# Kernel optimization log

Measured on AMD Instinct MI355X. Metric: run time of the kernel, lower is better.

Reference implementation:

```python
import jax, jax.numpy as jnp
import numpy as np

EMB = 512
HEADS = 8
USE_MASK = True


def setup_inputs() -> dict:
    key = jax.random.key(0)
    ks = jax.random.split(key, 6)
    b, t, e, h = 4, 1024, EMB, HEADS
    scale = 1.0 / np.sqrt(e)
    return {
        "x": jax.random.normal(ks[0], (b, t, e), dtype=jnp.float32),
        # nn.Linear(emb, emb*heads, bias=False) weights, stored as (out, in) like torch
        "w_k": jax.random.normal(ks[1], (e * h, e), dtype=jnp.float32) * scale,
        "w_q": jax.random.normal(ks[2], (e * h, e), dtype=jnp.float32) * scale,
        "w_v": jax.random.normal(ks[3], (e * h, e), dtype=jnp.float32) * scale,
        # unifyheads: Linear(heads*emb, emb) with bias
        "w_u": jax.random.normal(ks[4], (e, e * h), dtype=jnp.float32) * (1.0 / np.sqrt(e * h)),
        "b_u": jax.random.normal(ks[5], (e,), dtype=jnp.float32) * 0.01,
    }


def _attention(x, w_k, w_q, w_v, w_u, b_u):
    b, t, e = x.shape
    h = HEADS
    # projections: (b,t,e) @ (e, e*h) -> (b,t,h,e)  (per-head dim == emb, 'wide' heads)
    k = (x @ w_k.T).reshape(b, t, h, e)
    q = (x @ w_q.T).reshape(b, t, h, e)
    v = (x @ w_v.T).reshape(b, t, h, e)
    # scale q and k each by e^{-1/4} (equiv. to scores / sqrt(e))
    s = e ** (-0.25)
    q = q * s
    k = k * s
    # scores: (b,h,t,t)
    dot = jnp.einsum("bqhe,bkhe->bhqk", q, k)
    if USE_MASK:
        # mask strictly-upper triangle (future positions), diagonal kept
        causal = jnp.tril(jnp.ones((t, t), dtype=bool))
        dot = jnp.where(causal, dot, -jnp.inf)
    attn = jax.nn.softmax(dot, axis=-1)
    out = jnp.einsum("bhqk,bkhe->bqhe", attn, v).reshape(b, t, h * e)
    return out @ w_u.T + b_u


def reference(x, w_k, w_q, w_v, w_u, b_u):
    return _attention(x, w_k, w_q, w_v, w_u, b_u)
```

## Files before the change

### kernel.cpp

```cpp
#include <hip/hip_runtime.h>
#include <stdint.h>

typedef unsigned short u16;
typedef unsigned int u32;
typedef __bf16 bf16_t;
typedef __attribute__((ext_vector_type(8))) bf16_t bf16x8;
typedef __attribute__((ext_vector_type(4))) float floatx4;

__device__ __forceinline__ u16 f2b(float f) {
  u32 u = __float_as_uint(f);
  return (u16)((u + 0x7fffu + ((u >> 16) & 1u)) >> 16);
}

__device__ __forceinline__ void gload_lds16(const u16* g, u16* l) {
  __builtin_amdgcn_global_load_lds(
      (const __attribute__((address_space(1))) u32*)g,
      (__attribute__((address_space(3))) u32*)l, 16, 0, 0);
}

__global__ __launch_bounds__(256) void cvt_kernel(
    const float* __restrict__ s0, const float* __restrict__ s1,
    const float* __restrict__ s2, const float* __restrict__ s3,
    const float* __restrict__ s4, u16* __restrict__ dbase) {
  const int which = blockIdx.y;
  const float* s = which == 0 ? s0 : which == 1 ? s1 : which == 2 ? s2
                 : which == 3 ? s3 : s4;
  u16* d = dbase + (long)which * 2097152;
  const int i = blockIdx.x * 256 + threadIdx.x;
  const float4 v = ((const float4*)s)[i];
  ushort4 o;
  o.x = f2b(v.x); o.y = f2b(v.y); o.z = f2b(v.z); o.w = f2b(v.w);
  ((ushort4*)d)[i] = o;
}

__global__ __launch_bounds__(256) void init_out_kernel(float* __restrict__ out,
                                                       const float* __restrict__ bias) {
  const int i = blockIdx.x * 256 + threadIdx.x;
  const int c4 = i & 127;
  ((float4*)out)[i] = ((const float4*)bias)[c4];
}

enum { A_PLAIN = 0, A_HEADBLK = 1 };
enum { B_PLAIN = 0, B_TRANS = 1 };
enum { C_BF16_PLAIN = 0, C_BF16_BHTE = 1, C_F32_PLAIN = 2, C_F32_ATOMIC = 3 };

#define MFMA16(MB)                                                                                 \
  do {                                                                                             \
    acc[(MB) + 0][0] = __builtin_amdgcn_mfma_f32_16x16x32_bf16(A0, B0, acc[(MB) + 0][0], 0, 0, 0); \
    acc[(MB) + 0][1] = __builtin_amdgcn_mfma_f32_16x16x32_bf16(A0, B1, acc[(MB) + 0][1], 0, 0, 0); \
    acc[(MB) + 0][2] = __builtin_amdgcn_mfma_f32_16x16x32_bf16(A0, B2, acc[(MB) + 0][2], 0, 0, 0); \
    acc[(MB) + 0][3] = __builtin_amdgcn_mfma_f32_16x16x32_bf16(A0, B3, acc[(MB) + 0][3], 0, 0, 0); \
    acc[(MB) + 1][0] = __builtin_amdgcn_mfma_f32_16x16x32_bf16(A1, B0, acc[(MB) + 1][0], 0, 0, 0); \
    acc[(MB) + 1][1] = __builtin_amdgcn_mfma_f32_16x16x32_bf16(A1, B1, acc[(MB) + 1][1], 0, 0, 0); \
    acc[(MB) + 1][2] = __builtin_amdgcn_mfma_f32_16x16x32_bf16(A1, B2, acc[(MB) + 1][2], 0, 0, 0); \
    acc[(MB) + 1][3] = __builtin_amdgcn_mfma_f32_16x16x32_bf16(A1, B3, acc[(MB) + 1][3], 0, 0, 0); \
    acc[(MB) + 2][0] = __builtin_amdgcn_mfma_f32_16x16x32_bf16(A2, B0, acc[(MB) + 2][0], 0, 0, 0); \
    acc[(MB) + 2][1] = __builtin_amdgcn_mfma_f32_16x16x32_bf16(A2, B1, acc[(MB) + 2][1], 0, 0, 0); \
    acc[(MB) + 2][2] = __builtin_amdgcn_mfma_f32_16x16x32_bf16(A2, B2, acc[(MB) + 2][2], 0, 0, 0); \
    acc[(MB) + 2][3] = __builtin_amdgcn_mfma_f32_16x16x32_bf16(A2, B3, acc[(MB) + 2][3], 0, 0, 0); \
    acc[(MB) + 3][0] = __builtin_amdgcn_mfma_f32_16x16x32_bf16(A3, B0, acc[(MB) + 3][0], 0, 0, 0); \
    acc[(MB) + 3][1] = __builtin_amdgcn_mfma_f32_16x16x32_bf16(A3, B1, acc[(MB) + 3][1], 0, 0, 0); \
    acc[(MB) + 3][2] = __builtin_amdgcn_mfma_f32_16x16x32_bf16(A3, B2, acc[(MB) + 3][2], 0, 0, 0); \
    acc[(MB) + 3][3] = __builtin_amdgcn_mfma_f32_16x16x32_bf16(A3, B3, acc[(MB) + 3][3], 0, 0, 0); \
  } while (0)

#define STG_A(hn, c)                                                             \
  {                                                                              \
    const int kn_ = (hn) & 15;                                                   \
    gload_lds16(ag + (long)((c) << 7) * lda + (kn_ << 5),                        \
                &lds[(((kn_ >> 1) & 1) << 15) + ((kn_ & 1) << 13) + ((c) << 12) + ls]); \
  }
#define STG_B(hn, c)                                                             \
  {                                                                              \
    const int kn_ = (hn) & 15, zn_ = (hn) >> 4;                                  \
    gload_lds16(bg + (long)zn_ * b_zstride + (long)((c) << 7) * ldb + (kn_ << 5),\
                &lds[(((kn_ >> 1) & 1) << 15) + 16384 + ((kn_ & 1) << 13) + ((c) << 12) + ls]); \
  }

#define PHASE_SYNC_PRE()                                \
  __builtin_amdgcn_s_barrier();                         \
  asm volatile("s_waitcnt lgkmcnt(0)" ::: "memory");    \
  __builtin_amdgcn_sched_barrier(0);                    \
  __builtin_amdgcn_s_setprio(1)

#define PHASE_SYNC_POST()                               \
  __builtin_amdgcn_s_setprio(0);                        \
  __builtin_amdgcn_s_barrier();                         \
  __builtin_amdgcn_sched_barrier(0)

#define HALF_ITER(kk, hn, DO_STAGE, VM)                               \
  {                                                                   \
    const int slab_ = ((((kk) >> 1) & 1) << 15) + (((kk) & 1) << 13); \
    const u16* la_ = &lds[slab_ + ard];                               \
    const u16* lb_ = &lds[slab_ + brd];                               \
    A0 = *(const bf16x8*)(la_ + 0 * 512);                             \
    A1 = *(const bf16x8*)(la_ + 1 * 512);                             \
    A2 = *(const bf16x8*)(la_ + 2 * 512);                             \
    A3 = *(const bf16x8*)(la_ + 3 * 512);                             \
    B0 = *(const bf16x8*)(lb_ + 0 * 512);                             \
    B1 = *(const bf16x8*)(lb_ + 1 * 512);                             \
    B2 = *(const bf16x8*)(lb_ + 2 * 512);                             \
    B3 = *(const bf16x8*)(lb_ + 3 * 512);                             \
    if (DO_STAGE) { STG_A((hn), 0); STG_A((hn), 1); }                 \
    PHASE_SYNC_PRE();                                                 \
    MFMA16(0);                                                        \
    PHASE_SYNC_POST();                                                \
    A0 = *(const bf16x8*)(la_ + 4 * 512);                             \
    A1 = *(const bf16x8*)(la_ + 5 * 512);                             \
    A2 = *(const bf16x8*)(la_ + 6 * 512);                             \
    A3 = *(const bf16x8*)(la_ + 7 * 512);                             \
    if (DO_STAGE) { STG_B((hn), 0); STG_B((hn), 1); }                 \
    PHASE_SYNC_PRE();                                                 \
    MFMA16(4);                                                        \
    __builtin_amdgcn_s_setprio(0);                                    \
    asm volatile("s_waitcnt vmcnt(" #VM ")" ::: "memory");            \
    __builtin_amdgcn_s_barrier();                                     \
    __builtin_amdgcn_sched_barrier(0);                                \
  }

__global__ __launch_bounds__(512, 2) void gemm256_kernel(
    const u16* __restrict__ A, int lda,
    const u16* __restrict__ B, int ldb, long b_zstride,
    u16* __restrict__ C, long c_zstride) {
  __shared__ u16 lds[65536];

  const int tid = threadIdx.x;
  const int wid = tid >> 6, lane = tid & 63;
  const int lrow = lane & 15, quad = lane >> 4;
  const int wm = wid >> 2, wn = wid & 3;

  const int o = blockIdx.x;
  const int xcd = o & 7, j = o >> 3;
  const int m0 = (((xcd >> 1) << 2) | (j >> 3)) << 8;
  const int n0 = (((xcd & 1) << 3) | (j & 7)) << 8;

  const int scol = (((lane & 3) ^ ((lane >> 3) & 3)) << 3);
  const u16* ag = A + (long)(m0 + (wid << 4) + (lane >> 2)) * lda + scol;
  const u16* bg = B + (long)(n0 + (wid << 4) + (lane >> 2)) * ldb + scol;
  const int ls = wid << 9;

  const int qsw = ((quad ^ ((lrow >> 1) & 3)) << 3);
  const int ard = (((wm << 7) + lrow) << 5) + qsw;
  const int brd = 16384 + (((wn << 6) + lrow) << 5) + qsw;

  floatx4 acc[8][4];
#pragma unroll
  for (int i = 0; i < 8; ++i)
#pragma unroll
    for (int jj = 0; jj < 4; ++jj) acc[i][jj] = (floatx4)0.0f;

  STG_A(0, 0); STG_A(0, 1); STG_B(0, 0); STG_B(0, 1);
  STG_A(1, 0); STG_A(1, 1); STG_B(1, 0); STG_B(1, 1);
  STG_A(2, 0); STG_A(2, 1); STG_B(2, 0); STG_B(2, 1);
  asm volatile("s_waitcnt vmcnt(8)" ::: "memory");
  __builtin_amdgcn_s_barrier();
  __builtin_amdgcn_sched_barrier(0);

  bf16x8 A0, A1, A2, A3, B0, B1, B2, B3;

  for (int z = 0; z < 3; ++z) {
    const int hb = z << 4;
    if (z < 2) {
      for (int kk = 0; kk < 16; ++kk) HALF_ITER(kk, hb + kk + 3, true, 8);
    } else {
      for (int kk = 0; kk < 13; ++kk) HALF_ITER(kk, hb + kk + 3, true, 8);
      HALF_ITER(13, 0, false, 4);
      HALF_ITER(14, 0, false, 0);
      {
        const int slab_ = 32768 + 8192;
        const u16* la_ = &lds[slab_ + ard];
        const u16* lb_ = &lds[slab_ + brd];
        A0 = *(const bf16x8*)(la_ + 0 * 512);
        A1 = *(const bf16x8*)(la_ + 1 * 512);
        A2 = *(const bf16x8*)(la_ + 2 * 512);
        A3 = *(const bf16x8*)(la_ + 3 * 512);
        B0 = *(const bf16x8*)(lb_ + 0 * 512);
        B1 = *(const bf16x8*)(lb_ + 1 * 512);
        B2 = *(const bf16x8*)(lb_ + 2 * 512);
        B3 = *(const bf16x8*)(lb_ + 3 * 512);
        PHASE_SYNC_PRE();
        MFMA16(0);
        PHASE_SYNC_POST();
        A0 = *(const bf16x8*)(la_ + 4 * 512);
        A1 = *(const bf16x8*)(la_ + 5 * 512);
        A2 = *(const bf16x8*)(la_ + 6 * 512);
        A3 = *(const bf16x8*)(la_ + 7 * 512);
        PHASE_SYNC_PRE();
        MFMA16(4);
        __builtin_amdgcn_s_setprio(0);
      }
    }

#pragma unroll
    for (int mi = 0; mi < 8; ++mi) {
#pragma unroll
      for (int ni = 0; ni < 4; ++ni) {
        const int cg = n0 + (wn << 6) + (ni << 4) + lrow;
        const long cbase = (long)z * c_zstride + (long)(cg >> 9) * 524288 + (cg & 511);
#pragma unroll
        for (int r = 0; r < 4; ++r) {
          const int rg = m0 + (wm << 7) + (mi << 4) + (quad << 2) + r;
          C[cbase + (long)(rg >> 10) * 4194304 + (long)(rg & 1023) * 512] = f2b(acc[mi][ni][r]);
        }
        acc[mi][ni] = (floatx4)0.0f;
      }
    }
  }
}

__global__ __launch_bounds__(256) void vt_kernel(const u16* __restrict__ V,
                                                 u16* __restrict__ VT) {
  __shared__ u16 tl[4096];
  const long base = (long)blockIdx.z * 524288;
  const int t0 = blockIdx.x << 6, e0 = blockIdx.y << 6;
  const int tid = threadIdx.x;
  const int r = tid >> 3, g = tid & 7;
#pragma unroll
  for (int h = 0; h < 2; ++h) {
    const int row = r + (h << 5);
    const uint4 v = *(const uint4*)&V[base + (long)(t0 + row) * 512 + e0 + (g << 3)];
    *(uint4*)&tl[(row << 6) + ((g ^ (row & 7)) << 3)] = v;
  }
  __syncthreads();
#pragma unroll
  for (int h = 0; h < 2; ++h) {
    const int el = r + (h << 5);
    union { u16 us[8]; uint4 v; } o;
#pragma unroll
    for (int j = 0; j < 8; ++j) {
      const int trow = (g << 3) + j;
      o.us[j] = tl[(trow << 6) + ((((el >> 3) ^ (trow & 7)) << 3) + (el & 7))];
    }
    *(uint4*)&VT[base + (long)(e0 + el) * 1024 + t0 + (g << 3)] = o.v;
  }
}

#define FS_STG(es)                                                          \
  {                                                                         \
    const int sl_ = (es) % 3;                                               \
    gload_lds16(qgq + (es) * 64, &lds[sl_ * 12288 + ls]);                   \
    gload_lds16(kgj + (es) * 64, &lds[sl_ * 12288 + 4096 + ls]);            \
    gload_lds16(kgj + (es) * 64 + 32, &lds[sl_ * 12288 + 8192 + ls]);       \
  }
#define FV_STG(c)                                                           \
  {                                                                         \
    const int vb_ = 45056 + ((c) & 1) * 16384;                              \
    const u16* vgc_ = vgj + (c) * 131072;                                   \
    gload_lds16(vgc_, &lds[vb_ + ls]);                                      \
    gload_lds16(vgc_ + 32, &lds[vb_ + 4096 + ls]);                          \
    gload_lds16(vgc_ + 64, &lds[vb_ + 8192 + ls]);                          \
    gload_lds16(vgc_ + 96, &lds[vb_ + 12288 + ls]);                         \
  }

__global__ __launch_bounds__(512, 2) void flash_kernel(
    const u16* __restrict__ Qg, const u16* __restrict__ Kg,
    const u16* __restrict__ VTg, u16* __restrict__ Og) {
  __shared__ u16 lds[77824];

  const int tid = threadIdx.x;
  const int wid = tid >> 6, lane = tid & 63;
  const int lrow = lane & 15, quad = lane >> 4;
  const int wm = wid >> 2, wn = wid & 3;

  const int blk = blockIdx.x;
  const int bh = ((blk & 7) << 2) | ((blk >> 3) & 3);
  const int pr = blk >> 5;

  const long base = (long)bh * 524288;
  const u16* Qb = Qg + base;
  const u16* Kb = Kg + base;
  const u16* Vb = VTg + base;
  u16* Ob = Og + base;

  const int scol = (((lane & 3) ^ ((lane >> 3) & 3)) << 3);
  const int ls = wid << 9;
  const int qsw = ((quad ^ ((lrow >> 1) & 3)) << 3);

  const u16* qg0 = Qb + (long)(((wid & 3) << 4) + (lane >> 2)) * 512 + ((wid >> 2) << 5) + scol;
  const u16* kg0 = Kb + (long)((wid << 4) + (lane >> 2)) * 512 + scol;
  const u16* vg0 = Vb + (long)((wid << 4) + (lane >> 2)) * 1024 + scol;

  const int a_rd = ((wm << 5) + lrow) * 32 + qsw;
  const int b_rd = ((wn << 5) + lrow) * 32 + qsw;
  const int p_rd = 36864 + ((wm << 5) + lrow) * 32 + qsw;
  float* red_max = (float*)lds;
  float* red_sum = ((float*)lds) + 256;
  const float s2 = 0.044194173824159216f;

  for (int ht = 0; ht < 2; ++ht) {
    const int qt = ht ? (15 - pr) : pr;
    const int q0 = qt << 6;
    const int nk = (qt >> 1) + 1;
    const u16* qgq = qg0 + (long)q0 * 512;

    floatx4 oa[2][4][2];
#pragma unroll
    for (int a = 0; a < 2; ++a)
#pragma unroll
      for (int b = 0; b < 4; ++b)
#pragma unroll
        for (int c = 0; c < 2; ++c) oa[a][b][c] = (floatx4)0.0f;
    float m_st[2][4], l_st[2][4];
#pragma unroll
    for (int a = 0; a < 2; ++a)
#pragma unroll
      for (int r = 0; r < 4; ++r) { m_st[a][r] = -3.0e38f; l_st[a][r] = 0.0f; }

    for (int j = 0; j < nk; ++j) {
      const int k0 = j << 7;
      const bool maskt = (j == nk - 1);
      const u16* kgj = kg0 + (long)k0 * 512;
      const u16* vgj = vg0 + k0;

      floatx4 sacc[2][2];
      sacc[0][0] = sacc[0][1] = sacc[1][0] = sacc[1][1] = (floatx4)0.0f;

      FS_STG(0); FS_STG(1);
      asm volatile("s_waitcnt vmcnt(3)" ::: "memory");
      __builtin_amdgcn_s_barrier();
      __builtin_amdgcn_sched_barrier(0);
#pragma unroll
      for (int es = 0; es < 8; ++es) {
        const int sb = (es % 3) * 12288;
        bf16x8 qa[2][2], kb[2][2];
#pragma unroll
        for (int ks = 0; ks < 2; ++ks) {
#pragma unroll
          for (int mi = 0; mi < 2; ++mi)
            qa[ks][mi] = *(const bf16x8*)&lds[sb + ks * 2048 + a_rd + mi * 512];
#pragma unroll
          for (int ni = 0; ni < 2; ++ni)
            kb[ks][ni] = *(const bf16x8*)&lds[sb + 4096 + ks * 4096 + b_rd + ni * 512];
        }
        if (es < 6) FS_STG(es + 2);
        __builtin_amdgcn_s_barrier();
        asm volatile("s_waitcnt lgkmcnt(0)" ::: "memory");
        __builtin_amdgcn_sched_barrier(0);
        __builtin_amdgcn_s_setprio(1);
#pragma unroll
        for (int ks = 0; ks < 2; ++ks)
#pragma unroll
          for (int mi = 0; mi < 2; ++mi)
#pragma unroll
            for (int ni = 0; ni < 2; ++ni)
              sacc[mi][ni] = __builtin_amdgcn_mfma_f32_16x16x32_bf16(
                  qa[ks][mi], kb[ks][ni], sacc[mi][ni], 0, 0, 0);
        __builtin_amdgcn_s_setprio(0);
        if (es < 6) { asm volatile("s_waitcnt vmcnt(3)" ::: "memory"); }
        else if (es == 6) { asm volatile("s_waitcnt vmcnt(0)" ::: "memory"); }
        __builtin_amdgcn_s_barrier();
        __builtin_amdgcn_sched_barrier(0);
      }

      FV_STG(0); FV_STG(1);

      float sv[2][2][4];
#pragma unroll
      for (int mi = 0; mi < 2; ++mi)
#pragma unroll
        for (int ni = 0; ni < 2; ++ni)
#pragma unroll
          for (int r = 0; r < 4; ++r) {
            float s = sacc[mi][ni][r] * s2;
            if (maskt) {
              const int kc = k0 + (wn << 5) + (ni << 4) + lrow;
              const int qr = q0 + (wm << 5) + (mi << 4) + (quad << 2) + r;
              if (kc > qr) s = -3.0e38f;
            }
            sv[mi][ni][r] = s;
          }
      float rm[2][4];
#pragma unroll
      for (int mi = 0; mi < 2; ++mi)
#pragma unroll
        for (int r = 0; r < 4; ++r) {
          float v = fmaxf(sv[mi][0][r], sv[mi][1][r]);
          v = fmaxf(v, __shfl_xor(v, 1));
          v = fmaxf(v, __shfl_xor(v, 2));
          v = fmaxf(v, __shfl_xor(v, 4));
          v = fmaxf(v, __shfl_xor(v, 8));
          rm[mi][r] = v;
        }
      if (lrow == 0) {
#pragma unroll
        for (int mi = 0; mi < 2; ++mi)
#pragma unroll
          for (int r = 0; r < 4; ++r)
            red_max[(((wm << 5) + (mi << 4) + (quad << 2) + r) << 2) + wn] = rm[mi][r];
      }
      asm volatile("s_waitcnt lgkmcnt(0)" ::: "memory");
      __builtin_amdgcn_s_barrier();
      float mnew[2][4], resc[2][4];
#pragma unroll
      for (int mi = 0; mi < 2; ++mi)
#pragma unroll
        for (int r = 0; r < 4; ++r) {
          const float4 v4 =
              *(const float4*)&red_max[(((wm << 5) + (mi << 4) + (quad << 2) + r) << 2)];
          const float tm = fmaxf(fmaxf(v4.x, v4.y), fmaxf(v4.z, v4.w));
          const float mn = fmaxf(m_st[mi][r], tm);
          mnew[mi][r] = mn;
          resc[mi][r] = __expf(m_st[mi][r] - mn);
          m_st[mi][r] = mn;
        }
      float ps[2][4];
#pragma unroll
      for (int mi = 0; mi < 2; ++mi)
#pragma unroll
        for (int r = 0; r < 4; ++r) {
          const float p0 = __expf(sv[mi][0][r] - mnew[mi][r]);
          const float p1 = __expf(sv[mi][1][r] - mnew[mi][r]);
          sv[mi][0][r] = p0;
          sv[mi][1][r] = p1;
          float v = p0 + p1;
          v += __shfl_xor(v, 1);
          v += __shfl_xor(v, 2);
          v += __shfl_xor(v, 4);
          v += __shfl_xor(v, 8);
          ps[mi][r] = v;
        }
      if (lrow == 0) {
#pragma unroll
        for (int mi = 0; mi < 2; ++mi)
#pragma unroll
          for (int r = 0; r < 4; ++r)
            red_sum[(((wm << 5) + (mi << 4) + (quad << 2) + r) << 2) + wn] = ps[mi][r];
      }
#pragma unroll
      for (int mi = 0; mi < 2; ++mi)
#pragma unroll
        for (int c = 0; c < 4; ++c)
#pragma unroll
          for (int n2 = 0; n2 < 2; ++n2)
#pragma unroll
            for (int r = 0; r < 4; ++r) oa[mi][c][n2][r] *= resc[mi][r];
      asm volatile("s_waitcnt lgkmcnt(0)" ::: "memory");
      __builtin_amdgcn_s_barrier();
#pragma unroll
      for (int mi = 0; mi < 2; ++mi)
#pragma unroll
        for (int r = 0; r < 4; ++r) {
          const float4 v4 =
              *(const float4*)&red_sum[(((wm << 5) + (mi << 4) + (quad << 2) + r) << 2)];
          l_st[mi][r] = l_st[mi][r] * resc[mi][r] + (v4.x + v4.y + v4.z + v4.w);
        }
#pragma unroll
      for (int mi = 0; mi < 2; ++mi)
#pragma unroll
        for (int ni = 0; ni < 2; ++ni)
#pragma unroll
          for (int r = 0; r < 4; ++r) {
            const int qrow = (wm << 5) + (mi << 4) + (quad << 2) + r;
            const int c32 = (ni << 4) + lrow;
            const int slot = (c32 >> 3) ^ ((qrow >> 1) & 3);
            lds[36864 + (wn << 11) + qrow * 32 + (slot << 3) + (c32 & 7)] =
                f2b(sv[mi][ni][r]);
          }
      asm volatile("s_waitcnt lgkmcnt(0)" ::: "memory");
      asm volatile("s_waitcnt vmcnt(4)" ::: "memory");
      __builtin_amdgcn_s_barrier();
      __builtin_amdgcn_sched_barrier(0);

      bf16x8 pa[2][4];
#pragma unroll
      for (int mi = 0; mi < 2; ++mi)
#pragma unroll
        for (int ks = 0; ks < 4; ++ks)
          pa[mi][ks] = *(const bf16x8*)&lds[p_rd + mi * 512 + ks * 2048];
#pragma unroll
      for (int c = 0; c < 4; ++c) {
        const int vb0 = 45056 + (c & 1) * 16384;
        bf16x8 vb[2][4];
#pragma unroll
        for (int n2 = 0; n2 < 2; ++n2)
#pragma unroll
          for (int ks = 0; ks < 4; ++ks)
            vb[n2][ks] = *(const bf16x8*)&lds[vb0 + ks * 4096 + b_rd + n2 * 512];
        asm volatile("s_waitcnt lgkmcnt(0)" ::: "memory");
        __builtin_amdgcn_sched_barrier(0);
        __builtin_amdgcn_s_barrier();
        if (c < 2) FV_STG(c + 2);
        __builtin_amdgcn_s_setprio(1);
#pragma unroll
        for (int ks = 0; ks < 4; ++ks)
#pragma unroll
          for (int mi = 0; mi < 2; ++mi)
#pragma unroll
            for (int n2 = 0; n2 < 2; ++n2)
              oa[mi][c][n2] = __builtin_amdgcn_mfma_f32_16x16x32_bf16(
                  pa[mi][ks], vb[n2][ks], oa[mi][c][n2], 0, 0, 0);
        __builtin_amdgcn_s_setprio(0);
        if (c < 2) { asm volatile("s_waitcnt vmcnt(4)" ::: "memory"); }
        else if (c == 2) { asm volatile("s_waitcnt vmcnt(0)" ::: "memory"); }
        __builtin_amdgcn_s_barrier();
        __builtin_amdgcn_sched_barrier(0);
      }
    }

    float inv[2][4];
#pragma unroll
    for (int mi = 0; mi < 2; ++mi)
#pragma unroll
      for (int r = 0; r < 4; ++r) inv[mi][r] = 1.0f / l_st[mi][r];
#pragma unroll
    for (int mi = 0; mi < 2; ++mi)
#pragma unroll
      for (int c = 0; c < 4; ++c)
#pragma unroll
        for (int n2 = 0; n2 < 2; ++n2)
#pragma unroll
          for (int r = 0; r < 4; ++r) {
            const int trow = q0 + (wm << 5) + (mi << 4) + (quad << 2) + r;
            const int e = (c << 7) + (wn << 5) + (n2 << 4) + lrow;
            Ob[(long)trow * 512 + e] = f2b(oa[mi][c][n2][r] * inv[mi][r]);
          }
  }
}

template <int AMODE, int BMODE, int CMODE, bool CAUSAL_SKIP, bool PV_KLIM, bool HAS_BIAS,
          bool SPLITK>
__global__ __launch_bounds__(256, 2) void gemm_kernel(
    const u16* __restrict__ A, int lda, long a_zstride,
    const u16* __restrict__ B, int ldb, long b_zstride,
    void* __restrict__ C, int ldc, long c_zstride,
    const float* __restrict__ bias, int K, float scale) {
  const int bn = blockIdx.x, bm = blockIdx.y, bz = blockIdx.z;
  if (CAUSAL_SKIP && bn > bm) return;

  int kTiles = K >> 5;
  if (PV_KLIM) kTiles = (bm + 1) * 4;
  const int kbase = SPLITK ? bz * K : 0;

  const u16* Ab = A + (SPLITK ? 0 : (long)bz * a_zstride);
  const u16* Bb = B + (SPLITK ? 0 : (long)bz * b_zstride);

  constexpr int BSTR = (BMODE == B_TRANS) ? 40 : 32;
  __shared__ u16 sA[128 * 32];
  __shared__ u16 sB[128 * BSTR];

  const int tid = threadIdx.x;
  const int wid = tid >> 6;
  const int lane = tid & 63;
  const int lrow = lane & 15;
  const int quad = lane >> 4;
  const int wm = wid >> 1, wn = wid & 1;
  const int m0 = bm * 128, n0 = bn * 128;

  const int sgr = lane >> 2;
  const int sgc = (lane & 3) << 3;

  floatx4 acc[4][4];
#pragma unroll
  for (int i = 0; i < 4; ++i)
#pragma unroll
    for (int j = 0; j < 4; ++j) acc[i][j] = (floatx4)0.0f;

  for (int kt = 0; kt < kTiles; ++kt) {
    const int k0 = kbase + (kt << 5);
#pragma unroll
    for (int j = 0; j < 2; ++j) {
      const int r = wid * 32 + j * 16 + sgr;
      const u16* g;
      if constexpr (AMODE == A_PLAIN) {
        g = Ab + (long)(m0 + r) * lda + (k0 + sgc);
      } else {
        const int rg = m0 + r, kg = k0 + sgc;
        g = Ab + (long)((rg >> 10) * 8 + (kg >> 9)) * 524288 +
            (long)(rg & 1023) * 512 + (kg & 511);
      }
      gload_lds16(g, &sA[(wid * 32 + j * 16) * 32]);
    }
    if constexpr (BMODE == B_PLAIN) {
#pragma unroll
      for (int j = 0; j < 2; ++j) {
        const int r = wid * 32 + j * 16 + sgr;
        const u16* g = Bb + (long)(n0 + r) * ldb + (k0 + sgc);
        gload_lds16(g, &sB[(wid * 32 + j * 16) * 32]);
      }
    } else {
      const int tr = tid & 31, te = (tid >> 5) << 4;
      const u16* g = Bb + (long)(k0 + tr) * ldb + (n0 + te);
      union { uint4 v[2]; u16 s[16]; } tmp;
      tmp.v[0] = *(const uint4*)g;
      tmp.v[1] = *(const uint4*)(g + 8);
#pragma unroll
      for (int i = 0; i < 16; ++i) sB[(te + i) * BSTR + tr] = tmp.s[i];
    }
    __syncthreads();

    bf16x8 af[4], bfr[4];
#pragma unroll
    for (int i = 0; i < 4; ++i)
      af[i] = *(const bf16x8*)&sA[(wm * 64 + i * 16 + lrow) * 32 + (quad << 3)];
#pragma unroll
    for (int i = 0; i < 4; ++i)
      bfr[i] = *(const bf16x8*)&sB[(wn * 64 + i * 16 + lrow) * BSTR + (quad << 3)];
#pragma unroll
    for (int mi = 0; mi < 4; ++mi)
#pragma unroll
      for (int ni = 0; ni < 4; ++ni)
        acc[mi][ni] = __builtin_amdgcn_mfma_f32_16x16x32_bf16(af[mi], bfr[ni], acc[mi][ni], 0, 0, 0);
    __syncthreads();
  }

#pragma unroll
  for (int mi = 0; mi < 4; ++mi) {
#pragma unroll
    for (int ni = 0; ni < 4; ++ni) {
      const int cg = n0 + wn * 64 + ni * 16 + lrow;
      float bv = 0.0f;
      if constexpr (HAS_BIAS) bv = bias[cg];
#pragma unroll
      for (int r = 0; r < 4; ++r) {
        const int rg = m0 + wm * 64 + mi * 16 + quad * 4 + r;
        const float val = acc[mi][ni][r] * scale + bv;
        if constexpr (CMODE == C_F32_PLAIN) {
          ((float*)C)[(long)bz * c_zstride + (long)rg * ldc + cg] = val;
        } else if constexpr (CMODE == C_F32_ATOMIC) {
          atomicAdd(&((float*)C)[(long)rg * ldc + cg], val);
        } else if constexpr (CMODE == C_BF16_PLAIN) {
          ((u16*)C)[(long)bz * c_zstride + (long)rg * ldc + cg] = f2b(val);
        } else {
          const long idx = (long)bz * c_zstride +
                           (long)((rg >> 10) * 8 + (cg >> 9)) * 524288 +
                           (long)(rg & 1023) * 512 + (cg & 511);
          ((u16*)C)[idx] = f2b(val);
        }
      }
    }
  }
}

extern "C" void kernel_launch(void* const* d_in, const int* in_sizes, int n_in,
                              void* d_out, int out_size, void* d_ws, size_t ws_size,
                              hipStream_t stream) {
  const float* x   = (const float*)d_in[0];
  const float* w_k = (const float*)d_in[1];
  const float* w_q = (const float*)d_in[2];
  const float* w_v = (const float*)d_in[3];
  const float* w_u = (const float*)d_in[4];
  const float* b_u = (const float*)d_in[5];
  float* out = (float*)d_out;
  char* ws = (char*)d_ws;

  const long MB = 1048576;
  u16* xb  = (u16*)(ws);
  u16* wqb = (u16*)(ws + 4 * MB);
  u16* wub = (u16*)(ws + 16 * MB);
  u16* Q   = (u16*)(ws + 20 * MB);
  u16* Kb  = (u16*)(ws + 52 * MB);
  u16* V   = (u16*)(ws + 84 * MB);
  u16* O   = (u16*)(ws + 116 * MB);
  u16* VT  = (u16*)(ws + 148 * MB);

  const dim3 blk(256);

  cvt_kernel<<<dim3(2048, 5), blk, 0, stream>>>(x, w_q, w_k, w_v, w_u, xb);

  gemm256_kernel<<<dim3(256), dim3(512), 0, stream>>>(
      xb, 512, wqb, 512, 2097152, Q, 16777216);

  vt_kernel<<<dim3(16, 8, 32), blk, 0, stream>>>(V, VT);

  flash_kernel<<<dim3(256), dim3(512), 0, stream>>>(Q, Kb, VT, O);

  init_out_kernel<<<2048, blk, 0, stream>>>(out, b_u);
  gemm_kernel<A_HEADBLK, B_PLAIN, C_F32_ATOMIC, false, false, false, true>
      <<<dim3(4, 32, 4), blk, 0, stream>>>(O, 0, 0, wub, 4096, 0, out, 512, 0,
                                           nullptr, 1024, 1.0f);
}
```

Baseline: 312.2 us.

## Enlarge flash attention Q tile to 128 rows and drop paired-tile scheduling

The flash kernel now processes one 128-row query tile per block, where before each block handled two 64-row tiles in a balanced pair (pr and 15-pr). Each K/V chunk loaded into LDS is now reused across twice as many query rows, and the LDS layout is reorganized with a smaller total footprint. Register pressure rises because the O accumulator and softmax state double, and causal load balance gets worse, since blocks now do between 1 and 8 key tiles. Grid size still depends on the launch code, which is not visible here.

```diff
diff --git a/kernel.cpp b/kernel.cpp
--- a/kernel.cpp
+++ b/kernel.cpp
@@ -235,27 +235,28 @@
   }
 }
 
-#define FS_STG(es)                                                          \
-  {                                                                         \
-    const int sl_ = (es) % 3;                                               \
-    gload_lds16(qgq + (es) * 64, &lds[sl_ * 12288 + ls]);                   \
-    gload_lds16(kgj + (es) * 64, &lds[sl_ * 12288 + 4096 + ls]);            \
-    gload_lds16(kgj + (es) * 64 + 32, &lds[sl_ * 12288 + 8192 + ls]);       \
-  }
-#define FV_STG(c)                                                           \
-  {                                                                         \
-    const int vb_ = 45056 + ((c) & 1) * 16384;                              \
-    const u16* vgc_ = vgj + (c) * 131072;                                   \
-    gload_lds16(vgc_, &lds[vb_ + ls]);                                      \
-    gload_lds16(vgc_ + 32, &lds[vb_ + 4096 + ls]);                          \
-    gload_lds16(vgc_ + 64, &lds[vb_ + 8192 + ls]);                          \
-    gload_lds16(vgc_ + 96, &lds[vb_ + 12288 + ls]);                         \
+#define FS3(es)                                                            \
+  {                                                                        \
+    const int sl_ = ((es) % 3) * 16384;                                    \
+    gload_lds16(qgq + (es) * 64, &lds[sl_ + ls]);                          \
+    gload_lds16(qgq + (es) * 64 + 32, &lds[sl_ + 4096 + ls]);              \
+    gload_lds16(kgj + (es) * 64, &lds[sl_ + 8192 + ls]);                   \
+    gload_lds16(kgj + (es) * 64 + 32, &lds[sl_ + 12288 + ls]);             \
+  }
+#define FV3(c)                                                             \
+  {                                                                        \
+    const int vb_ = ((c) & 1) << 14;                                       \
+    const u16* vgc_ = vgj + (c) * 131072;                                  \
+    gload_lds16(vgc_, &lds[vb_ + ls]);                                     \
+    gload_lds16(vgc_ + 32, &lds[vb_ + 4096 + ls]);                         \
+    gload_lds16(vgc_ + 64, &lds[vb_ + 8192 + ls]);                         \
+    gload_lds16(vgc_ + 96, &lds[vb_ + 12288 + ls]);                        \
   }
 
 __global__ __launch_bounds__(512, 2) void flash_kernel(
     const u16* __restrict__ Qg, const u16* __restrict__ Kg,
     const u16* __restrict__ VTg, u16* __restrict__ Og) {
-  __shared__ u16 lds[77824];
+  __shared__ u16 lds[67584];
 
   const int tid = threadIdx.x;
   const int wid = tid >> 6, lane = tid & 63;
@@ -264,7 +265,9 @@
 
   const int blk = blockIdx.x;
   const int bh = ((blk & 7) << 2) | ((blk >> 3) & 3);
-  const int pr = blk >> 5;
+  const int qt = blk >> 5;
+  const int q0 = qt << 7;
+  const int nk = qt + 1;
 
   const long base = (long)bh * 524288;
   const u16* Qb = Qg + base;
@@ -276,245 +279,235 @@
   const int ls = wid << 9;
   const int qsw = ((quad ^ ((lrow >> 1) & 3)) << 3);
 
-  const u16* qg0 = Qb + (long)(((wid & 3) << 4) + (lane >> 2)) * 512 + ((wid >> 2) << 5) + scol;
+  const u16* qgq = Qb + (long)(q0 + (wid << 4) + (lane >> 2)) * 512 + scol;
   const u16* kg0 = Kb + (long)((wid << 4) + (lane >> 2)) * 512 + scol;
   const u16* vg0 = Vb + (long)((wid << 4) + (lane >> 2)) * 1024 + scol;
 
-  const int a_rd = ((wm << 5) + lrow) * 32 + qsw;
-  const int b_rd = ((wn << 5) + lrow) * 32 + qsw;
-  const int p_rd = 36864 + ((wm << 5) + lrow) * 32 + qsw;
-  float* red_max = (float*)lds;
-  float* red_sum = ((float*)lds) + 256;
+  const int a_rd = ((wm << 6) + lrow) * 32 + qsw;
+  const int k_rd = ((wn << 5) + lrow) * 32 + qsw;
+  const int p_rd = 49152 + ((wm << 6) + lrow) * 32 + qsw;
+  float* red_max = (float*)&lds[65536];
+  float* red_sum = red_max + 512;
   const float s2 = 0.044194173824159216f;
 
-  for (int ht = 0; ht < 2; ++ht) {
-    const int qt = ht ? (15 - pr) : pr;
-    const int q0 = qt << 6;
-    const int nk = (qt >> 1) + 1;
-    const u16* qgq = qg0 + (long)q0 * 512;
-
-    floatx4 oa[2][4][2];
-#pragma unroll
-    for (int a = 0; a < 2; ++a)
-#pragma unroll
-      for (int b = 0; b < 4; ++b)
-#pragma unroll
-        for (int c = 0; c < 2; ++c) oa[a][b][c] = (floatx4)0.0f;
-    float m_st[2][4], l_st[2][4];
-#pragma unroll
-    for (int a = 0; a < 2; ++a)
-#pragma unroll
-      for (int r = 0; r < 4; ++r) { m_st[a][r] = -3.0e38f; l_st[a][r] = 0.0f; }
-
-    for (int j = 0; j < nk; ++j) {
-      const int k0 = j << 7;
-      const bool maskt = (j == nk - 1);
-      const u16* kgj = kg0 + (long)k0 * 512;
-      const u16* vgj = vg0 + k0;
-
-      floatx4 sacc[2][2];
-      sacc[0][0] = sacc[0][1] = sacc[1][0] = sacc[1][1] = (floatx4)0.0f;
-
-      FS_STG(0); FS_STG(1);
-      asm volatile("s_waitcnt vmcnt(3)" ::: "memory");
+  floatx4 oa[4][4][2];
+#pragma unroll
+  for (int a = 0; a < 4; ++a)
+#pragma unroll
+    for (int b = 0; b < 4; ++b)
+#pragma unroll
+      for (int c = 0; c < 2; ++c) oa[a][b][c] = (floatx4)0.0f;
+  float m_st[4][4], l_st[4][4];
+#pragma unroll
+  for (int a = 0; a < 4; ++a)
+#pragma unroll
+    for (int r = 0; r < 4; ++r) { m_st[a][r] = -3.0e38f; l_st[a][r] = 0.0f; }
+
+  for (int j = 0; j < nk; ++j) {
+    const int k0 = j << 7;
+    const bool mk = (j == nk - 1);
+    const u16* kgj = kg0 + (long)k0 * 512;
+    const u16* vgj = vg0 + k0;
+
+    floatx4 sacc[4][2];
+#pragma unroll
+    for (int mi = 0; mi < 4; ++mi) { sacc[mi][0] = (floatx4)0.0f; sacc[mi][1] = (floatx4)0.0f; }
+
+    FS3(0); FS3(1);
+    asm volatile("s_waitcnt vmcnt(4)" ::: "memory");
+    __builtin_amdgcn_s_barrier();
+    __builtin_amdgcn_sched_barrier(0);
+#pragma unroll
+    for (int es = 0; es < 8; ++es) {
+      const int sb = (es % 3) * 16384;
+      if (es < 6) FS3(es + 2);
       __builtin_amdgcn_s_barrier();
       __builtin_amdgcn_sched_barrier(0);
-#pragma unroll
-      for (int es = 0; es < 8; ++es) {
-        const int sb = (es % 3) * 12288;
-        bf16x8 qa[2][2], kb[2][2];
-#pragma unroll
-        for (int ks = 0; ks < 2; ++ks) {
-#pragma unroll
-          for (int mi = 0; mi < 2; ++mi)
-            qa[ks][mi] = *(const bf16x8*)&lds[sb + ks * 2048 + a_rd + mi * 512];
+      __builtin_amdgcn_s_setprio(1);
+#pragma unroll
+      for (int ks = 0; ks < 2; ++ks) {
+        bf16x8 qa[4], kb[2];
+#pragma unroll
+        for (int mi = 0; mi < 4; ++mi)
+          qa[mi] = *(const bf16x8*)&lds[sb + ks * 4096 + a_rd + mi * 512];
+#pragma unroll
+        for (int ni = 0; ni < 2; ++ni)
+          kb[ni] = *(const bf16x8*)&lds[sb + 8192 + ks * 4096 + k_rd + ni * 512];
+#pragma unroll
+        for (int mi = 0; mi < 4; ++mi)
 #pragma unroll
           for (int ni = 0; ni < 2; ++ni)
-            kb[ks][ni] = *(const bf16x8*)&lds[sb + 4096 + ks * 4096 + b_rd + ni * 512];
-        }
-        if (es < 6) FS_STG(es + 2);
-        __builtin_amdgcn_s_barrier();
-        asm volatile("s_waitcnt lgkmcnt(0)" ::: "memory");
-        __builtin_amdgcn_sched_barrier(0);
-        __builtin_amdgcn_s_setprio(1);
-#pragma unroll
-        for (int ks = 0; ks < 2; ++ks)
-#pragma unroll
-          for (int mi = 0; mi < 2; ++mi)
-#pragma unroll
-            for (int ni = 0; ni < 2; ++ni)
-              sacc[mi][ni] = __builtin_amdgcn_mfma_f32_16x16x32_bf16(
-                  qa[ks][mi], kb[ks][ni], sacc[mi][ni], 0, 0, 0);
-        __builtin_amdgcn_s_setprio(0);
-        if (es < 6) { asm volatile("s_waitcnt vmcnt(3)" ::: "memory"); }
-        else if (es == 6) { asm volatile("s_waitcnt vmcnt(0)" ::: "memory"); }
-        __builtin_amdgcn_s_barrier();
-        __builtin_amdgcn_sched_barrier(0);
-      }
-
-      FV_STG(0); FV_STG(1);
-
-      float sv[2][2][4];
-#pragma unroll
-      for (int mi = 0; mi < 2; ++mi)
-#pragma unroll
-        for (int ni = 0; ni < 2; ++ni)
-#pragma unroll
-          for (int r = 0; r < 4; ++r) {
-            float s = sacc[mi][ni][r] * s2;
-            if (maskt) {
-              const int kc = k0 + (wn << 5) + (ni << 4) + lrow;
-              const int qr = q0 + (wm << 5) + (mi << 4) + (quad << 2) + r;
-              if (kc > qr) s = -3.0e38f;
-            }
-            sv[mi][ni][r] = s;
-          }
-      float rm[2][4];
-#pragma unroll
-      for (int mi = 0; mi < 2; ++mi)
-#pragma unroll
-        for (int r = 0; r < 4; ++r) {
-          float v = fmaxf(sv[mi][0][r], sv[mi][1][r]);
-          v = fmaxf(v, __shfl_xor(v, 1));
-          v = fmaxf(v, __shfl_xor(v, 2));
-          v = fmaxf(v, __shfl_xor(v, 4));
-          v = fmaxf(v, __shfl_xor(v, 8));
-          rm[mi][r] = v;
-        }
-      if (lrow == 0) {
-#pragma unroll
-        for (int mi = 0; mi < 2; ++mi)
-#pragma unroll
-          for (int r = 0; r < 4; ++r)
-            red_max[(((wm << 5) + (mi << 4) + (quad << 2) + r) << 2) + wn] = rm[mi][r];
-      }
-      asm volatile("s_waitcnt lgkmcnt(0)" ::: "memory");
-      __builtin_amdgcn_s_barrier();
-      float mnew[2][4], resc[2][4];
-#pragma unroll
-      for (int mi = 0; mi < 2; ++mi)
-#pragma unroll
-        for (int r = 0; r < 4; ++r) {
-          const float4 v4 =
-              *(const float4*)&red_max[(((wm << 5) + (mi << 4) + (quad << 2) + r) << 2)];
-          const float tm = fmaxf(fmaxf(v4.x, v4.y), fmaxf(v4.z, v4.w));
-          const float mn = fmaxf(m_st[mi][r], tm);
-          mnew[mi][r] = mn;
-          resc[mi][r] = __expf(m_st[mi][r] - mn);
-          m_st[mi][r] = mn;
-        }
-      float ps[2][4];
-#pragma unroll
-      for (int mi = 0; mi < 2; ++mi)
-#pragma unroll
-        for (int r = 0; r < 4; ++r) {
-          const float p0 = __expf(sv[mi][0][r] - mnew[mi][r]);
-          const float p1 = __expf(sv[mi][1][r] - mnew[mi][r]);
-          sv[mi][0][r] = p0;
-          sv[mi][1][r] = p1;
-          float v = p0 + p1;
-          v += __shfl_xor(v, 1);
-          v += __shfl_xor(v, 2);
-          v += __shfl_xor(v, 4);
-          v += __shfl_xor(v, 8);
-          ps[mi][r] = v;
-        }
-      if (lrow == 0) {
-#pragma unroll
-        for (int mi = 0; mi < 2; ++mi)
-#pragma unroll
-          for (int r = 0; r < 4; ++r)
-            red_sum[(((wm << 5) + (mi << 4) + (quad << 2) + r) << 2) + wn] = ps[mi][r];
-      }
-#pragma unroll
-      for (int mi = 0; mi < 2; ++mi)
-#pragma unroll
-        for (int c = 0; c < 4; ++c)
-#pragma unroll
-          for (int n2 = 0; n2 < 2; ++n2)
-#pragma unroll
-            for (int r = 0; r < 4; ++r) oa[mi][c][n2][r] *= resc[mi][r];
-      asm volatile("s_waitcnt lgkmcnt(0)" ::: "memory");
-      __builtin_amdgcn_s_barrier();
-#pragma unroll
-      for (int mi = 0; mi < 2; ++mi)
-#pragma unroll
-        for (int r = 0; r < 4; ++r) {
-          const float4 v4 =
-              *(const float4*)&red_sum[(((wm << 5) + (mi << 4) + (quad << 2) + r) << 2)];
-          l_st[mi][r] = l_st[mi][r] * resc[mi][r] + (v4.x + v4.y + v4.z + v4.w);
-        }
-#pragma unroll
-      for (int mi = 0; mi < 2; ++mi)
-#pragma unroll
-        for (int ni = 0; ni < 2; ++ni)
-#pragma unroll
-          for (int r = 0; r < 4; ++r) {
-            const int qrow = (wm << 5) + (mi << 4) + (quad << 2) + r;
-            const int c32 = (ni << 4) + lrow;
-            const int slot = (c32 >> 3) ^ ((qrow >> 1) & 3);
-            lds[36864 + (wn << 11) + qrow * 32 + (slot << 3) + (c32 & 7)] =
-                f2b(sv[mi][ni][r]);
-          }
-      asm volatile("s_waitcnt lgkmcnt(0)" ::: "memory");
-      asm volatile("s_waitcnt vmcnt(4)" ::: "memory");
+            sacc[mi][ni] = __builtin_amdgcn_mfma_f32_16x16x32_bf16(
+                qa[mi], kb[ni], sacc[mi][ni], 0, 0, 0);
+      }
+      __builtin_amdgcn_s_setprio(0);
+      if (es < 6) { asm volatile("s_waitcnt vmcnt(4)" ::: "memory"); }
+      else if (es == 6) { asm volatile("s_waitcnt vmcnt(0)" ::: "memory"); }
       __builtin_amdgcn_s_barrier();
       __builtin_amdgcn_sched_barrier(0);
-
-      bf16x8 pa[2][4];
-#pragma unroll
-      for (int mi = 0; mi < 2; ++mi)
+    }
+
+    FV3(0); FV3(1);
+
+    float sv[4][2][4];
+#pragma unroll
+    for (int mi = 0; mi < 4; ++mi)
+#pragma unroll
+      for (int ni = 0; ni < 2; ++ni)
+#pragma unroll
+        for (int r = 0; r < 4; ++r) {
+          float s = sacc[mi][ni][r] * s2;
+          if (mk) {
+            const int kc = k0 + (wn << 5) + (ni << 4) + lrow;
+            const int qr = q0 + (wm << 6) + (mi << 4) + (quad << 2) + r;
+            if (kc > qr) s = -3.0e38f;
+          }
+          sv[mi][ni][r] = s;
+        }
+    float rm[4][4];
+#pragma unroll
+    for (int mi = 0; mi < 4; ++mi)
+#pragma unroll
+      for (int r = 0; r < 4; ++r) {
+        float v = fmaxf(sv[mi][0][r], sv[mi][1][r]);
+        v = fmaxf(v, __shfl_xor(v, 1));
+        v = fmaxf(v, __shfl_xor(v, 2));
+        v = fmaxf(v, __shfl_xor(v, 4));
+        v = fmaxf(v, __shfl_xor(v, 8));
+        rm[mi][r] = v;
+      }
+    if (lrow == 0) {
+#pragma unroll
+      for (int mi = 0; mi < 4; ++mi)
+#pragma unroll
+        for (int r = 0; r < 4; ++r)
+          red_max[(((wm << 6) + (mi << 4) + (quad << 2) + r) << 2) + wn] = rm[mi][r];
+    }
+    asm volatile("s_waitcnt lgkmcnt(0)" ::: "memory");
+    __builtin_amdgcn_s_barrier();
+    float mnew[4][4], resc[4][4];
+#pragma unroll
+    for (int mi = 0; mi < 4; ++mi)
+#pragma unroll
+      for (int r = 0; r < 4; ++r) {
+        const float4 v4 =
+            *(const float4*)&red_max[(((wm << 6) + (mi << 4) + (quad << 2) + r) << 2)];
+        const float tm = fmaxf(fmaxf(v4.x, v4.y), fmaxf(v4.z, v4.w));
+        const float mn = fmaxf(m_st[mi][r], tm);
+        mnew[mi][r] = mn;
+        resc[mi][r] = __expf(m_st[mi][r] - mn);
+        m_st[mi][r] = mn;
+      }
+    float ps[4][4];
+#pragma unroll
+    for (int mi = 0; mi < 4; ++mi)
+#pragma unroll
+      for (int r = 0; r < 4; ++r) {
+        const float p0 = __expf(sv[mi][0][r] - mnew[mi][r]);
+        const float p1 = __expf(sv[mi][1][r] - mnew[mi][r]);
+        sv[mi][0][r] = p0;
+        sv[mi][1][r] = p1;
+        float v = p0 + p1;
+        v += __shfl_xor(v, 1);
+        v += __shfl_xor(v, 2);
+        v += __shfl_xor(v, 4);
+        v += __shfl_xor(v, 8);
+        ps[mi][r] = v;
+      }
+    if (lrow == 0) {
+#pragma unroll
+      for (int mi = 0; mi < 4; ++mi)
+#pragma unroll
+        for (int r = 0; r < 4; ++r)
+          red_sum[(((wm << 6) + (mi << 4) + (quad << 2) + r) << 2) + wn] = ps[mi][r];
+    }
+#pragma unroll
+    for (int mi = 0; mi < 4; ++mi)
+#pragma unroll
+      for (int c = 0; c < 4; ++c)
+#pragma unroll
+        for (int n2 = 0; n2 < 2; ++n2)
+#pragma unroll
+          for (int r = 0; r < 4; ++r) oa[mi][c][n2][r] *= resc[mi][r];
+    asm volatile("s_waitcnt lgkmcnt(0)" ::: "memory");
+    __builtin_amdgcn_s_barrier();
+#pragma unroll
+    for (int mi = 0; mi < 4; ++mi)
+#pragma unroll
+      for (int r = 0; r < 4; ++r) {
+        const float4 v4 =
+            *(const float4*)&red_sum[(((wm << 6) + (mi << 4) + (quad << 2) + r) << 2)];
+        l_st[mi][r] = l_st[mi][r] * resc[mi][r] + (v4.x + v4.y + v4.z + v4.w);
+      }
+#pragma unroll
+    for (int mi = 0; mi < 4; ++mi)
+#pragma unroll
+      for (int ni = 0; ni < 2; ++ni)
+#pragma unroll
+        for (int r = 0; r < 4; ++r) {
+          const int qrow = (wm << 6) + (mi << 4) + (quad << 2) + r;
+          const int c32 = (ni << 4) + lrow;
+          const int slot = (c32 >> 3) ^ ((qrow >> 1) & 3);
+          lds[49152 + (wn << 12) + qrow * 32 + (slot << 3) + (c32 & 7)] =
+              f2b(sv[mi][ni][r]);
+        }
+    asm volatile("s_waitcnt lgkmcnt(0)" ::: "memory");
+    asm volatile("s_waitcnt vmcnt(4)" ::: "memory");
+    __builtin_amdgcn_s_barrier();
+    __builtin_amdgcn_sched_barrier(0);
+
+#pragma unroll
+    for (int c = 0; c < 4; ++c) {
+      const int vb0 = (c & 1) << 14;
+      bf16x8 vb[2][4];
+#pragma unroll
+      for (int n2 = 0; n2 < 2; ++n2)
 #pragma unroll
         for (int ks = 0; ks < 4; ++ks)
-          pa[mi][ks] = *(const bf16x8*)&lds[p_rd + mi * 512 + ks * 2048];
-#pragma unroll
-      for (int c = 0; c < 4; ++c) {
-        const int vb0 = 45056 + (c & 1) * 16384;
-        bf16x8 vb[2][4];
-#pragma unroll
-        for (int n2 = 0; n2 < 2; ++n2)
-#pragma unroll
-          for (int ks = 0; ks < 4; ++ks)
-            vb[n2][ks] = *(const bf16x8*)&lds[vb0 + ks * 4096 + b_rd + n2 * 512];
-        asm volatile("s_waitcnt lgkmcnt(0)" ::: "memory");
-        __builtin_amdgcn_sched_barrier(0);
-        __builtin_amdgcn_s_barrier();
-        if (c < 2) FV_STG(c + 2);
-        __builtin_amdgcn_s_setprio(1);
-#pragma unroll
-        for (int ks = 0; ks < 4; ++ks)
-#pragma unroll
-          for (int mi = 0; mi < 2; ++mi)
-#pragma unroll
-            for (int n2 = 0; n2 < 2; ++n2)
-              oa[mi][c][n2] = __builtin_amdgcn_mfma_f32_16x16x32_bf16(
-                  pa[mi][ks], vb[n2][ks], oa[mi][c][n2], 0, 0, 0);
-        __builtin_amdgcn_s_setprio(0);
-        if (c < 2) { asm volatile("s_waitcnt vmcnt(4)" ::: "memory"); }
-        else if (c == 2) { asm volatile("s_waitcnt vmcnt(0)" ::: "memory"); }
-        __builtin_amdgcn_s_barrier();
-        __builtin_amdgcn_sched_barrier(0);
-      }
-    }
-
-    float inv[2][4];
-#pragma unroll
-    for (int mi = 0; mi < 2; ++mi)
-#pragma unroll
-      for (int r = 0; r < 4; ++r) inv[mi][r] = 1.0f / l_st[mi][r];
-#pragma unroll
-    for (int mi = 0; mi < 2; ++mi)
-#pragma unroll
-      for (int c = 0; c < 4; ++c)
-#pragma unroll
-        for (int n2 = 0; n2 < 2; ++n2)
-#pragma unroll
-          for (int r = 0; r < 4; ++r) {
-            const int trow = q0 + (wm << 5) + (mi << 4) + (quad << 2) + r;
-            const int e = (c << 7) + (wn << 5) + (n2 << 4) + lrow;
-            Ob[(long)trow * 512 + e] = f2b(oa[mi][c][n2][r] * inv[mi][r]);
-          }
-  }
+          vb[n2][ks] = *(const bf16x8*)&lds[vb0 + ks * 4096 + k_rd + n2 * 512];
+      asm volatile("s_waitcnt lgkmcnt(0)" ::: "memory");
+      __builtin_amdgcn_sched_barrier(0);
+      __builtin_amdgcn_s_barrier();
+      if (c < 2) FV3(c + 2);
+      __builtin_amdgcn_s_setprio(1);
+#pragma unroll
+      for (int ks = 0; ks < 4; ++ks) {
+        bf16x8 pa[4];
+#pragma unroll
+        for (int mi = 0; mi < 4; ++mi)
+          pa[mi] = *(const bf16x8*)&lds[p_rd + ks * 4096 + mi * 512];
+#pragma unroll
+        for (int mi = 0; mi < 4; ++mi)
+#pragma unroll
+          for (int n2 = 0; n2 < 2; ++n2)
+            oa[mi][c][n2] = __builtin_amdgcn_mfma_f32_16x16x32_bf16(
+                pa[mi], vb[n2][ks], oa[mi][c][n2], 0, 0, 0);
+      }
+      __builtin_amdgcn_s_setprio(0);
+      if (c < 2) { asm volatile("s_waitcnt vmcnt(4)" ::: "memory"); }
+      else if (c == 2) { asm volatile("s_waitcnt vmcnt(0)" ::: "memory"); }
+      __builtin_amdgcn_s_barrier();
+      __builtin_amdgcn_sched_barrier(0);
+    }
+  }
+
+  float inv[4][4];
+#pragma unroll
+  for (int mi = 0; mi < 4; ++mi)
+#pragma unroll
+    for (int r = 0; r < 4; ++r) inv[mi][r] = 1.0f / l_st[mi][r];
+#pragma unroll
+  for (int mi = 0; mi < 4; ++mi)
+#pragma unroll
+    for (int c = 0; c < 4; ++c)
+#pragma unroll
+      for (int n2 = 0; n2 < 2; ++n2)
+#pragma unroll
+        for (int r = 0; r < 4; ++r) {
+          const int trow = q0 + (wm << 6) + (mi << 4) + (quad << 2) + r;
+          const int e = (c << 7) + (wn << 5) + (n2 << 4) + lrow;
+          Ob[(long)trow * 512 + e] = f2b(oa[mi][c][n2][r] * inv[mi][r]);
+        }
 }
 
 template <int AMODE, int BMODE, int CMODE, bool CAUSAL_SKIP, bool PV_KLIM, bool HAS_BIAS,
```

After: 504.2 us. +61.5%, slower.
